# Performance work log

Hardware: AMD Instinct MI355X
Metric: run time of the kernel (lower is better)

Reference implementation:

```python
import jax, jax.numpy as jnp
import numpy as np

B = 262144      # batch of Monte Carlo paths
D = 5           # number of assets
NSTEPS = 20     # Euler-Maruyama steps
H = 0.1         # T / N
R = 0.06        # risk-free rate
T = 2.0
SIGMA = 0.2     # vol (same for all assets)
B_DRIFT = 0.1   # P-measure drift
CURTAGE = 0.005
SQRT_H = float(np.sqrt(H))


def setup_inputs() -> dict:
    key = jax.random.key(0)
    ks = jax.random.split(key, 10)
    sc = 0.1  # weight init scale
    return {
        "x_in": jax.random.uniform(ks[0], (B, 1), dtype=jnp.float32),
        "dW": jax.random.normal(ks[1], (NSTEPS, B, D), dtype=jnp.float32) * SQRT_H,
        "Wo": jax.random.normal(ks[2], (1, 2 * D + 1), dtype=jnp.float32) * sc,
        "bo": jnp.zeros((2 * D + 1,), jnp.float32),
        "Wk": jax.random.normal(ks[3], (1, 2 * D), dtype=jnp.float32) * sc,
        "bk": jnp.zeros((2 * D,), jnp.float32),
        "Wu0": jax.random.normal(ks[4], (1, D), dtype=jnp.float32) * sc,
        "bu0": jnp.zeros((D,), jnp.float32),
        "W1": jax.random.normal(ks[5], (NSTEPS - 1, 1, 20), dtype=jnp.float32) * sc,
        "b1": jnp.zeros((NSTEPS - 1, 20), jnp.float32),
        "W2": jax.random.normal(ks[6], (NSTEPS - 1, 20, 20), dtype=jnp.float32) * sc,
        "b2": jnp.zeros((NSTEPS - 1, 20), jnp.float32),
        "W3": jax.random.normal(ks[7], (NSTEPS - 1, 20, D), dtype=jnp.float32) * sc,
        "b3": jnp.zeros((NSTEPS - 1, D), jnp.float32),
    }


def _mlp(x, w1, c1, w2, c2, w3, c3):
    # SubNetwork: Dense(20) relu -> Dense(20) relu -> Dense(D) linear
    h1 = jax.nn.relu(x @ w1 + c1)
    h2 = jax.nn.relu(h1 @ w2 + c2)
    return h2 @ w3 + c3


def _forward(x_in, dW, Wo, bo, Wk, bk, Wu0, bu0, W1, b1, W2, b2, W3, b3):
    b_vec = jnp.full((D,), B_DRIFT, dtype=x_in.dtype)
    x = x_in                                             # wealth [B,1]
    alpha_options = jax.nn.softmax(x @ Wo + bo, axis=-1)[:, : 2 * D]
    alpha_options_tot = jnp.mean(jnp.sum(alpha_options, axis=1))
    K = 1.0 + 0.25 * jnp.tanh(x @ Wk + bk)               # strikes [B,2D]
    rescale = 1.0 - alpha_options_tot
    alpha = x @ Wu0 + bu0                                # linear head, [B,D]

    S = jnp.ones((x.shape[0], D), dtype=x.dtype)         # P-measure asset prices
    S_Q = S                                              # Q-measure asset prices
    dN_acu = jnp.zeros((x.shape[0], D), dtype=x.dtype)
    N_m1 = None

    for n in range(1, NSTEPS + 1):   # fixed small unrolled rollout
        u = alpha                                        # dollar allocation per asset
        N_p = u / S                                      # number of shares
        if n > 1:
            dN_acu = dN_acu + jnp.abs(N_p - N_m1)        # turnover accumulator
        N_m1 = N_p
        dWn = dW[n - 1]
        # wealth Euler step: risk-free on cash + risky exposure (GBM, no jumps)
        x = x + (x - jnp.sum(u, axis=1, keepdims=True)) * (R * H) \
              + jnp.sum(u * (b_vec * H + SIGMA * dWn), axis=1, keepdims=True)
        S = S * (1.0 + b_vec * H + SIGMA * dWn)
        S_Q = S_Q * (1.0 + R * H + SIGMA * dWn)
        if n < NSTEPS:
            alpha = _mlp(x, W1[n - 1], b1[n - 1], W2[n - 1], b2[n - 1],
                         W3[n - 1], b3[n - 1])

    dN = jnp.sum(dN_acu, axis=1, keepdims=True)          # [B,1]
    disc = jnp.exp(-R * T)
    C0 = disc * jnp.mean(jnp.maximum(S_Q - K[:, :D], 0.0), axis=0)   # [D] MC call price
    P0 = disc * jnp.mean(jnp.maximum(K[:, D:] - S_Q, 0.0), axis=0)   # [D] MC put price
    C_T = jnp.maximum(S - K[:, :D], 0.0) / (C0 + 1e-8)
    P_T = jnp.maximum(K[:, D:] - S, 0.0) / (P0 + 1e-8)
    del P_T  # options_in_p=False: puts/calls not added to wealth

    x = x - CURTAGE * dN                                 # transaction costs

    p5 = jnp.percentile(x, 5.0)
    p95 = jnp.percentile(x, 95.0)
    m_lo = x < p5
    m_hi = x > p95
    cnt_lo = jnp.maximum(jnp.sum(m_lo), 1).astype(x.dtype)
    cnt_hi = jnp.maximum(jnp.sum(m_hi), 1).astype(x.dtype)

    loss1 = -jnp.mean(x)
    loss2 = jnp.var(x)
    loss3 = -jnp.sum(jnp.where(m_lo, x, 0.0)) / cnt_lo   # -CVaR_5 tail mean
    loss4 = -jnp.sum(jnp.where(m_hi, x, 0.0)) / cnt_hi
    loss5 = jnp.mean(C_T[:, 0])
    loss6 = K[0, 1]
    loss7 = jnp.asarray(rescale, x.dtype)
    return (loss1, loss2, loss3, loss4, loss5, loss6, loss7)


def reference(x_in, dW, Wo, bo, Wk, bk, Wu0, bu0, W1, b1, W2, b2, W3, b3):
    losses = _forward(x_in, dW, Wo, bo, Wk, bk, Wu0, bu0,
                      W1, b1, W2, b2, W3, b3)
    return tuple(jnp.reshape(l, (1,)) for l in losses)
```

## Files before the change

kernel.cpp:

```cpp
#include <hip/hip_runtime.h>
#include <math.h>

#define BB 262144
#define NST 20
#define RHc 0.006f
#define BHc 0.01f
#define SIGc 0.2f
#define CURTc 0.005f
#define DISCf 0.8869204367171575f

#define P 4
#define THB 256
#define NBLK_SIM 256
#define CH 65536

#define H1_BLK 32
#define H1_THR 1024
#define W_BLK 256
#define W_THR 256

#define SIMP_OFF  BB
#define TAILP_OFF (SIMP_OFF + NBLK_SIM * 5)
#define ICTRL     (TAILP_OFF + W_BLK * 4)
#define H2_OFF 0
#define H3_OFF 8192
#define CNT_OFF 12288
#define ST_OFF  12296
#define SF_OFF  12320
#define ZTOT    12289
#define H1R_OFF 12352

__device__ __forceinline__ unsigned fkey(float f) {
    unsigned u = __float_as_uint(f);
    return (u & 0x80000000u) ? ~u : (u | 0x80000000u);
}
__device__ __forceinline__ float funkey(unsigned k) {
    return __uint_as_float((k & 0x80000000u) ? (k ^ 0x80000000u) : ~k);
}
__device__ __forceinline__ float wred(float v) {
#pragma unroll
    for (int o = 32; o > 0; o >>= 1) v += __shfl_down(v, o);
    return v;
}
__device__ __forceinline__ unsigned short f2bf(float f) {
    unsigned u = __float_as_uint(f);
    unsigned r = u + 0x7fffu + ((u >> 16) & 1u);
    return (unsigned short)(r >> 16);
}

__global__ void zero_kernel(int* __restrict__ ctrl) {
    int i = blockIdx.x * blockDim.x + threadIdx.x;
    if (i < ZTOT) ctrl[i] = 0;
}

#define STRD 416
#define HB   (19 * STRD)

__global__ __launch_bounds__(THB, 1) void sim_kernel(
    const float* __restrict__ x_in, const float* __restrict__ dW,
    const float* __restrict__ Wo, const float* __restrict__ bo,
    const float* __restrict__ Wk, const float* __restrict__ bk,
    const float* __restrict__ Wu0, const float* __restrict__ bu0,
    const float* __restrict__ W1, const float* __restrict__ b1,
    const float* __restrict__ W2, const float* __restrict__ b2,
    const float* __restrict__ W3, const float* __restrict__ b3,
    float* __restrict__ ws, int* __restrict__ ctrl, float* __restrict__ out)
{
    __shared__ float L[HB + 40];
    __shared__ float red[4][5];
    __shared__ int lastF;
    const int tid = threadIdx.x;

    for (int t = tid; t < 19 * 20; t += THB) {
        int s = t / 20, j = t % 20;
        L[s * STRD + j]      = W1[t];
        L[s * STRD + 20 + j] = b1[t];
        L[s * STRD + 40 + j] = b2[t];
    }
    for (int t = tid; t < 19 * 100; t += THB) {
        int s = t / 100, r = t % 100, i = r / 5, k = r % 5;
        L[s * STRD + 60 + k * 20 + i] = W3[t];
    }
    for (int t = tid; t < 19 * 5; t += THB) {
        int s = t / 5, k = t % 5;
        L[s * STRD + 160 + k] = b3[t];
    }
    {
        unsigned short* Ls16 = (unsigned short*)L;
        for (int t = tid; t < 19 * 400; t += THB) {
            int s = t / 400, r = t % 400, i = r / 20, j = r % 20;
            Ls16[(s * STRD + 168 + i * 12) * 2 + j] = f2bf(W2[t]);
        }
        for (int t = tid; t < 19 * 80; t += THB) {
            int s = t / 80, r = t % 80, i = r / 4, q = r % 4;
            Ls16[(s * STRD + 168 + i * 12) * 2 + 20 + q] = 0;
        }
    }
    if (tid < 11) { L[HB + tid] = Wo[tid]; L[HB + 11 + tid] = bo[tid]; }
    if (tid == 0) { L[HB + 22] = Wk[0]; L[HB + 23] = bk[0]; }
    if (tid < 5)  { L[HB + 24 + tid] = Wu0[tid]; L[HB + 29 + tid] = bu0[tid]; }
    __syncthreads();

    const int b0 = blockIdx.x * THB + tid;

    float x[P], K0[P], SQ0[P], dNs[P], smv = 0.f;
    float alpha[P][5], S[P][5], Nm1[P][5], dwb[P][5];

#pragma unroll
    for (int p = 0; p < P; p++) {
        int b = b0 + p * CH;
        float xx = x_in[b];
        x[p] = xx;
        float z[11], zm = -1e30f;
#pragma unroll
        for (int j = 0; j < 11; j++) {
            z[j] = fmaf(xx, L[HB + j], L[HB + 11 + j]);
            zm = fmaxf(zm, z[j]);
        }
        float se = 0.f;
#pragma unroll
        for (int j = 0; j < 11; j++) se += __expf(z[j] - zm);
        smv += __expf(z[10] - zm) / se;
        K0[p] = 1.f + 0.25f * tanhf(fmaf(xx, L[HB + 22], L[HB + 23]));
        SQ0[p] = 1.f; dNs[p] = 0.f;
#pragma unroll
        for (int d = 0; d < 5; d++) {
            alpha[p][d] = fmaf(xx, L[HB + 24 + d], L[HB + 29 + d]);
            S[p][d] = 1.f;
            Nm1[p][d] = alpha[p][d];
        }
        const float* pw = dW + (size_t)b * 5;
#pragma unroll
        for (int d = 0; d < 5; d++) dwb[p][d] = pw[d];
    }

#pragma unroll 1
    for (int n = 1; n <= NST; n++) {
        float dwc[P][5];
#pragma unroll
        for (int p = 0; p < P; p++)
#pragma unroll
            for (int d = 0; d < 5; d++) dwc[p][d] = dwb[p][d];
        if (n < NST) {
#pragma unroll
            for (int p = 0; p < P; p++) {
                const float* pw = dW + ((size_t)n * BB + b0 + p * CH) * 5;
#pragma unroll
                for (int d = 0; d < 5; d++) dwb[p][d] = pw[d];
            }
        }
#pragma unroll
        for (int p = 0; p < P; p++) {
            float usum = 0.f, du = 0.f, dn = 0.f;
#pragma unroll
            for (int d = 0; d < 5; d++) {
                float u = alpha[p][d];
                float Np = u * __builtin_amdgcn_rcpf(S[p][d]);
                dn += fabsf(Np - Nm1[p][d]);
                Nm1[p][d] = Np;
                usum += u;
                du = fmaf(u, fmaf(SIGc, dwc[p][d], BHc), du);
            }
            dNs[p] += dn;
            x[p] = fmaf(x[p] - usum, RHc, x[p]) + du;
#pragma unroll
            for (int d = 0; d < 5; d++)
                S[p][d] *= (1.f + BHc + SIGc * dwc[p][d]);
            SQ0[p] *= (1.f + RHc + SIGc * dwc[p][0]);
        }
        if (n < NST) {
            const float* Ls = L + (n - 1) * STRD;
            float h2[P][20];
#pragma unroll
            for (int j4 = 0; j4 < 5; j4++) {
                float4 c = *(const float4*)(Ls + 40 + j4 * 4);
#pragma unroll
                for (int p = 0; p < P; p++) {
                    h2[p][j4 * 4 + 0] = c.x; h2[p][j4 * 4 + 1] = c.y;
                    h2[p][j4 * 4 + 2] = c.z; h2[p][j4 * 4 + 3] = c.w;
                }
            }
#pragma unroll 1
            for (int i4 = 0; i4 < 5; i4++) {
                float4 w1c = *(const float4*)(Ls + i4 * 4);
                float4 c1c = *(const float4*)(Ls + 20 + i4 * 4);
#pragma unroll
                for (int ii = 0; ii < 4; ii++) {
                    int i = i4 * 4 + ii;
                    const uint4 q0 = *(const uint4*)(Ls + 168 + i * 12);
                    const uint4 q1 = *(const uint4*)(Ls + 168 + i * 12 + 4);
                    const uint2 q2 = *(const uint2*)(Ls + 168 + i * 12 + 8);
                    float w[20];
                    w[0]  = __uint_as_float(q0.x << 16); w[1]  = __uint_as_float(q0.x & 0xffff0000u);
                    w[2]  = __uint_as_float(q0.y << 16); w[3]  = __uint_as_float(q0.y & 0xffff0000u);
                    w[4]  = __uint_as_float(q0.z << 16); w[5]  = __uint_as_float(q0.z & 0xffff0000u);
                    w[6]  = __uint_as_float(q0.w << 16); w[7]  = __uint_as_float(q0.w & 0xffff0000u);
                    w[8]  = __uint_as_float(q1.x << 16); w[9]  = __uint_as_float(q1.x & 0xffff0000u);
                    w[10] = __uint_as_float(q1.y << 16); w[11] = __uint_as_float(q1.y & 0xffff0000u);
                    w[12] = __uint_as_float(q1.z << 16); w[13] = __uint_as_float(q1.z & 0xffff0000u);
                    w[14] = __uint_as_float(q1.w << 16); w[15] = __uint_as_float(q1.w & 0xffff0000u);
                    w[16] = __uint_as_float(q2.x << 16); w[17] = __uint_as_float(q2.x & 0xffff0000u);
                    w[18] = __uint_as_float(q2.y << 16); w[19] = __uint_as_float(q2.y & 0xffff0000u);
                    float wv = (ii == 0) ? w1c.x : (ii == 1) ? w1c.y : (ii == 2) ? w1c.z : w1c.w;
                    float cv = (ii == 0) ? c1c.x : (ii == 1) ? c1c.y : (ii == 2) ? c1c.z : c1c.w;
#pragma unroll
                    for (int p = 0; p < P; p++) {
                        float hv = fmaxf(fmaf(x[p], wv, cv), 0.f);
#pragma unroll
                        for (int j = 0; j < 20; j++)
                            h2[p][j] = fmaf(hv, w[j], h2[p][j]);
                    }
                }
            }
#pragma unroll
            for (int p = 0; p < P; p++)
#pragma unroll
                for (int j = 0; j < 20; j++) h2[p][j] = fmaxf(h2[p][j], 0.f);
#pragma unroll
            for (int k = 0; k < 5; k++) {
                const float* wr = Ls + 60 + k * 20;
                float4 wa  = *(const float4*)(wr + 0);
                float4 wb2 = *(const float4*)(wr + 4);
                float4 wc2 = *(const float4*)(wr + 8);
                float4 wd2 = *(const float4*)(wr + 12);
                float4 we2 = *(const float4*)(wr + 16);
                float bb = Ls[160 + k];
#pragma unroll
                for (int p = 0; p < P; p++) {
                    float a = bb;
                    a = fmaf(h2[p][0], wa.x, a);  a = fmaf(h2[p][1], wa.y, a);
                    a = fmaf(h2[p][2], wa.z, a);  a = fmaf(h2[p][3], wa.w, a);
                    a = fmaf(h2[p][4], wb2.x, a); a = fmaf(h2[p][5], wb2.y, a);
                    a = fmaf(h2[p][6], wb2.z, a); a = fmaf(h2[p][7], wb2.w, a);
                    a = fmaf(h2[p][8], wc2.x, a); a = fmaf(h2[p][9], wc2.y, a);
                    a = fmaf(h2[p][10], wc2.z, a); a = fmaf(h2[p][11], wc2.w, a);
                    a = fmaf(h2[p][12], wd2.x, a); a = fmaf(h2[p][13], wd2.y, a);
                    a = fmaf(h2[p][14], wd2.z, a); a = fmaf(h2[p][15], wd2.w, a);
                    a = fmaf(h2[p][16], we2.x, a); a = fmaf(h2[p][17], we2.y, a);
                    a = fmaf(h2[p][18], we2.z, a); a = fmaf(h2[p][19], we2.w, a);
                    alpha[p][k] = a;
                }
            }
        }
    }

    float v0 = 0.f, v1 = 0.f, v2 = 0.f, v3 = 0.f, v4 = smv;
#pragma unroll
    for (int p = 0; p < P; p++) {
        float xx = fmaf(-CURTc, dNs[p], x[p]);
        ws[b0 + p * CH] = xx;
        v0 += xx; v1 += xx * xx;
        v2 += fmaxf(S[p][0] - K0[p], 0.f);
        v3 += fmaxf(SQ0[p]  - K0[p], 0.f);
    }

    v0 = wred(v0); v1 = wred(v1); v2 = wred(v2); v3 = wred(v3); v4 = wred(v4);
    int wid = tid >> 6, lane = tid & 63;
    if (lane == 0) { red[wid][0] = v0; red[wid][1] = v1; red[wid][2] = v2; red[wid][3] = v3; red[wid][4] = v4; }
    __syncthreads();
    if (tid == 0) {
        float s0 = 0, s1 = 0, s2 = 0, s3 = 0, s4 = 0;
#pragma unroll
        for (int w = 0; w < 4; w++) { s0 += red[w][0]; s1 += red[w][1]; s2 += red[w][2]; s3 += red[w][3]; s4 += red[w][4]; }
        float* part = ws + SIMP_OFF + blockIdx.x * 5;
        part[0] = s0; part[1] = s1; part[2] = s2; part[3] = s3; part[4] = s4;
    }
    __threadfence();
    if (tid == 0) lastF = (atomicAdd(&ctrl[CNT_OFF], 1) == NBLK_SIM - 1);
    __syncthreads();
    if (!lastF) return;
    __threadfence();

    const float* part = ws + SIMP_OFF;
    float a0 = part[tid * 5 + 0], a1 = part[tid * 5 + 1], a2 = part[tid * 5 + 2],
          a3 = part[tid * 5 + 3], a4 = part[tid * 5 + 4];
    a0 = wred(a0); a1 = wred(a1); a2 = wred(a2); a3 = wred(a3); a4 = wred(a4);
    if (lane == 0) { red[wid][0] = a0; red[wid][1] = a1; red[wid][2] = a2; red[wid][3] = a3; red[wid][4] = a4; }
    __syncthreads();
    if (tid == 0) {
        float Sx = 0, Sx2 = 0, SP = 0, SQs = 0, Ssm = 0;
#pragma unroll
        for (int w = 0; w < 4; w++) { Sx += red[w][0]; Sx2 += red[w][1]; SP += red[w][2]; SQs += red[w][3]; Ssm += red[w][4]; }
        float invB = 1.f / (float)BB;
        float meanx = Sx * invB;
        out[0] = -meanx;
        out[1] = Sx2 * invB - meanx * meanx;
        out[4] = (SP * invB) / (DISCf * (SQs * invB) + 1e-8f);
        out[5] = 1.f + 0.25f * tanhf(fmaf(x_in[0], Wk[1], bk[1]));
        out[6] = Ssm * invB;
    }
}

__device__ __forceinline__ void aggAdd(int* h, int code) {
    bool act = (code >= 0);
    unsigned long long mask = __ballot(act);
    while (mask) {
        int leader = __ffsll((unsigned long long)mask) - 1;
        int lc = __shfl(code, leader);
        unsigned long long mm = __ballot(act && code == lc);
        if ((threadIdx.x & 63) == leader) atomicAdd(&h[lc], (int)__popcll(mm));
        mask &= ~mm;
    }
}

__device__ int excl_scan1024(int v, int tid, int* wsum) {
    __syncthreads();
    int lane = tid & 63, wid = tid >> 6;
    int inc = v;
#pragma unroll
    for (int o = 1; o < 64; o <<= 1) { int u = __shfl_up(inc, o); if (lane >= o) inc += u; }
    if (lane == 63) wsum[wid] = inc;
    __syncthreads();
    if (tid < 16) {
        int wv = wsum[tid], winc = wv;
#pragma unroll
        for (int o = 1; o < 16; o <<= 1) { int u = __shfl_up(winc, o); if (tid >= o) winc += u; }
        wsum[tid] = winc - wv;
    }
    __syncthreads();
    return wsum[wid] + inc - v;
}

__global__ __launch_bounds__(H1_THR) void hist1_kernel(const float* __restrict__ xf,
                                                       int* __restrict__ ctrl)
{
    __shared__ int lh[2048];
    const int tid = threadIdx.x, bl = blockIdx.x;
    for (int i = tid; i < 2048; i += H1_THR) lh[i] = 0;
    __syncthreads();
    const float4* xf4 = (const float4*)xf;
#pragma unroll
    for (int w = 0; w < 2; w++) {
        float4 v = xf4[(size_t)bl * 2048 + w * 1024 + tid];
        aggAdd(lh, (int)(fkey(v.x) >> 21));
        aggAdd(lh, (int)(fkey(v.y) >> 21));
        aggAdd(lh, (int)(fkey(v.z) >> 21));
        aggAdd(lh, (int)(fkey(v.w) >> 21));
    }
    __syncthreads();
    int* row = ctrl + H1R_OFF + bl * 2048;
    for (int i = tid; i < 2048; i += H1_THR) row[i] = lh[i];
}

__global__ __launch_bounds__(1024) void scan1_kernel(int* __restrict__ ctrl)
{
    __shared__ int wsum[16];
    __shared__ int binT[4], remT[4];
    const int tid = threadIdx.x;
    const int* rows = ctrl + H1R_OFF;
    int c0 = 0, c1 = 0;
    for (int r = 0; r < H1_BLK; r++) {
        c0 += rows[r * 2048 + 2 * tid];
        c1 += rows[r * 2048 + 2 * tid + 1];
    }
    int s = c0 + c1;
    int E = excl_scan1024(s, tid, wsum);
    const int RK[4] = {13107, 13108, 249035, 249036};
#pragma unroll
    for (int t = 0; t < 4; t++) {
        int r = RK[t];
        if (r >= E && r < E + s) {
            if (r < E + c0) { binT[t] = 2 * tid;     remT[t] = r - E; }
            else            { binT[t] = 2 * tid + 1; remT[t] = r - E - c0; }
        }
    }
    __syncthreads();
    if (tid == 0) {
        for (int t = 0; t < 4; t++) { ctrl[ST_OFF + t] = binT[t]; ctrl[ST_OFF + 4 + t] = remT[t]; }
        for (int t = 0; t < 4; t++) {
            int g = t;
            for (int q = 0; q < t; q++) if (binT[q] == binT[t]) { g = q; break; }
            ctrl[ST_OFF + 8 + t] = g;
        }
    }
}

__global__ __launch_bounds__(W_THR) void hist2_kernel(const float* __restrict__ xf,
                                                      int* __restrict__ ctrl)
{
    const int tid = threadIdx.x, bl = blockIdx.x;
    int pf[4], gp[4];
#pragma unroll
    for (int t = 0; t < 4; t++) { pf[t] = ctrl[ST_OFF + t]; gp[t] = ctrl[ST_OFF + 8 + t]; }
    float4 v = ((const float4*)xf)[(size_t)bl * W_THR + tid];
    float xv[4] = {v.x, v.y, v.z, v.w};
#pragma unroll
    for (int k = 0; k < 4; k++) {
        unsigned u = fkey(xv[k]);
        unsigned hi = u >> 21;
        int bin = (int)((u >> 10) & 2047u);
        int code = -1;
#pragma unroll
        for (int t = 0; t < 4; t++)
            if (gp[t] == t && (unsigned)pf[t] == hi) code = t * 2048 + bin;
        aggAdd(ctrl + H2_OFF, code);
    }
}

__global__ __launch_bounds__(1024) void scan2_kernel(int* __restrict__ ctrl)
{
    __shared__ int wsum[16];
    __shared__ int binT[4], remT[4];
    const int tid = threadIdx.x;
    for (int t = 0; t < 4; t++) {
        int g = ctrl[ST_OFF + 8 + t], rank = ctrl[ST_OFF + 4 + t];
        const int* h = ctrl + H2_OFF + g * 2048;
        int c0 = h[2 * tid], c1 = h[2 * tid + 1];
        int s = c0 + c1;
        int E = excl_scan1024(s, tid, wsum);
        if (rank >= E && rank < E + s) {
            if (rank < E + c0) { binT[t] = 2 * tid;     remT[t] = rank - E; }
            else               { binT[t] = 2 * tid + 1; remT[t] = rank - E - c0; }
        }
        __syncthreads();
    }
    if (tid == 0) {
        int P2n[4];
        for (int t = 0; t < 4; t++) {
            P2n[t] = (ctrl[ST_OFF + t] << 11) | binT[t];
            ctrl[ST_OFF + 12 + t] = P2n[t];
            ctrl[ST_OFF + 16 + t] = remT[t];
        }
        for (int t = 0; t < 4; t++) {
            int g = t;
            for (int q = 0; q < t; q++) if (P2n[q] == P2n[t]) { g = q; break; }
            ctrl[ST_OFF + 20 + t] = g;
        }
    }
}

__global__ __launch_bounds__(W_THR) void hist3_kernel(const float* __restrict__ xf,
                                                      int* __restrict__ ctrl)
{
    const int tid = threadIdx.x, bl = blockIdx.x;
    int pf[4], gp[4];
#pragma unroll
    for (int t = 0; t < 4; t++) { pf[t] = ctrl[ST_OFF + 12 + t]; gp[t] = ctrl[ST_OFF + 20 + t]; }
    float4 v = ((const float4*)xf)[(size_t)bl * W_THR + tid];
    float xv[4] = {v.x, v.y, v.z, v.w};
#pragma unroll
    for (int k = 0; k < 4; k++) {
        unsigned u = fkey(xv[k]);
        unsigned hi = u >> 10;
        int bin = (int)(u & 1023u);
        int code = -1;
#pragma unroll
        for (int t = 0; t < 4; t++)
            if (gp[t] == t && (unsigned)pf[t] == hi) code = t * 1024 + bin;
        aggAdd(ctrl + H3_OFF, code);
    }
}

__global__ __launch_bounds__(1024) void scan3_kernel(int* __restrict__ ctrl)
{
    __shared__ int wsum[16];
    __shared__ int binT[4];
    const int tid = threadIdx.x;
    for (int t = 0; t < 4; t++) {
        int g = ctrl[ST_OFF + 20 + t], rank = ctrl[ST_OFF + 16 + t];
        const int* h = ctrl + H3_OFF + g * 1024;
        int s = h[tid];
        int E = excl_scan1024(s, tid, wsum);
        if (rank >= E && rank < E + s) binT[t] = tid;
        __syncthreads();
    }
    if (tid == 0) {
        float* sf = (float*)(ctrl + SF_OFF);
        float v[4];
        for (int t = 0; t < 4; t++) {
            unsigned key = ((unsigned)ctrl[ST_OFF + 12 + t] << 10) | (unsigned)binT[t];
            v[t] = funkey(key);
            sf[t] = v[t];
        }
        sf[4] = v[0] + 0.15f * (v[1] - v[0]);
        sf[5] = v[2] + 0.85f * (v[3] - v[2]);
    }
}

__global__ __launch_bounds__(W_THR) void tail_kernel(const float* __restrict__ xf,
                                                     const int* __restrict__ ctrl,
                                                     float* __restrict__ ws)
{
    __shared__ float frd[4][4];
    const int tid = threadIdx.x, bl = blockIdx.x;
    const float* sf = (const float*)(ctrl + SF_OFF);
    const float p5 = sf[4], p95 = sf[5];
    float4 v = ((const float4*)xf)[(size_t)bl * W_THR + tid];
    float xv[4] = {v.x, v.y, v.z, v.w};
    float slo = 0.f, clo = 0.f, shi = 0.f, chi = 0.f;
#pragma unroll
    for (int k = 0; k < 4; k++) {
        float x = xv[k];
        if (x < p5)  { slo += x; clo += 1.f; }
        if (x > p95) { shi += x; chi += 1.f; }
    }
    slo = wred(slo); clo = wred(clo); shi = wred(shi); chi = wred(chi);
    int wid = tid >> 6, lane = tid & 63;
    if (lane == 0) { frd[wid][0] = slo; frd[wid][1] = clo; frd[wid][2] = shi; frd[wid][3] = chi; }
    __syncthreads();
    if (tid == 0) {
        float s0 = 0, s1 = 0, s2 = 0, s3 = 0;
#pragma unroll
        for (int w = 0; w < 4; w++) { s0 += frd[w][0]; s1 += frd[w][1]; s2 += frd[w][2]; s3 += frd[w][3]; }
        float* tp = ws + TAILP_OFF + bl * 4;
        tp[0] = s0; tp[1] = s1; tp[2] = s2; tp[3] = s3;
    }
}

__global__ __launch_bounds__(256) void tailfin_kernel(const float* __restrict__ ws,
                                                      float* __restrict__ out)
{
    __shared__ float frd[4][4];
    const int tid = threadIdx.x;
    const float* tp = ws + TAILP_OFF;
    float a0 = tp[tid * 4 + 0], a1 = tp[tid * 4 + 1], a2 = tp[tid * 4 + 2], a3 = tp[tid * 4 + 3];
    a0 = wred(a0); a1 = wred(a1); a2 = wred(a2); a3 = wred(a3);
    int wid = tid >> 6, lane = tid & 63;
    if (lane == 0) { frd[wid][0] = a0; frd[wid][1] = a1; frd[wid][2] = a2; frd[wid][3] = a3; }
    __syncthreads();
    if (tid == 0) {
        float Slo = 0, Clo = 0, Shi = 0, Chi = 0;
#pragma unroll
        for (int w = 0; w < 4; w++) { Slo += frd[w][0]; Clo += frd[w][1]; Shi += frd[w][2]; Chi += frd[w][3]; }
        out[2] = -Slo / fmaxf(Clo, 1.f);
        out[3] = -Shi / fmaxf(Chi, 1.f);
    }
}

extern "C" void kernel_launch(void* const* d_in, const int* in_sizes, int n_in,
                              void* d_out, int out_size, void* d_ws, size_t ws_size,
                              hipStream_t stream)
{
    const float* x_in = (const float*)d_in[0];
    const float* dW   = (const float*)d_in[1];
    const float* Wo   = (const float*)d_in[2];
    const float* bo   = (const float*)d_in[3];
    const float* Wk   = (const float*)d_in[4];
    const float* bk   = (const float*)d_in[5];
    const float* Wu0  = (const float*)d_in[6];
    const float* bu0  = (const float*)d_in[7];
    const float* W1   = (const float*)d_in[8];
    const float* b1   = (const float*)d_in[9];
    const float* W2   = (const float*)d_in[10];
    const float* b2   = (const float*)d_in[11];
    const float* W3   = (const float*)d_in[12];
    const float* b3   = (const float*)d_in[13];
    float* ws  = (float*)d_ws;
    int* ctrl  = (int*)d_ws + ICTRL;
    float* out = (float*)d_out;

    zero_kernel<<<(ZTOT + 1023) / 1024, 1024, 0, stream>>>(ctrl);
    sim_kernel<<<NBLK_SIM, THB, 0, stream>>>(x_in, dW, Wo, bo, Wk, bk, Wu0, bu0,
                                             W1, b1, W2, b2, W3, b3, ws, ctrl, out);
    hist1_kernel<<<H1_BLK, H1_THR, 0, stream>>>(ws, ctrl);
    scan1_kernel<<<1, 1024, 0, stream>>>(ctrl);
    hist2_kernel<<<W_BLK, W_THR, 0, stream>>>(ws, ctrl);
    scan2_kernel<<<1, 1024, 0, stream>>>(ctrl);
    hist3_kernel<<<W_BLK, W_THR, 0, stream>>>(ws, ctrl);
    scan3_kernel<<<1, 1024, 0, stream>>>(ctrl);
    tail_kernel<<<W_BLK, W_THR, 0, stream>>>(ws, ctrl, ws);
    tailfin_kernel<<<1, 256, 0, stream>>>(ws, out);
}
```

Baseline: 192.1 us.

## Run per-step MLP layers on bf16 MFMA with pre-packed weight fragments

The per-path scalar FMA MLP (20x20 and 20x5 layers in LDS-bf16) is replaced by 32x32x16 bf16 MFMA instructions, with two half-waves splitting the five asset dimensions. A new prep kernel packs W2/W3/biases into MFMA fragment layouts in global memory, and the sim kernel now uses one path per lane-pair with many more blocks instead of four paths per thread. Hidden activations are also rounded to bf16, which adds precision loss, and the extra kernel launch and wider grid change the reduction and histogram partitioning.

```diff
diff --git a/kernel.cpp b/kernel.cpp
--- a/kernel.cpp
+++ b/kernel.cpp
@@ -1,4 +1,5 @@
 #include <hip/hip_runtime.h>
+#include <hip/hip_bf16.h>
 #include <math.h>
 
 #define BB 262144
@@ -9,12 +10,9 @@
 #define CURTc 0.005f
 #define DISCf 0.8869204367171575f
 
-#define P 4
 #define THB 256
-#define NBLK_SIM 256
-#define CH 65536
-
-#define H1_BLK 32
+#define NBLK_SIM 2048
+#define H1_BLK 16
 #define H1_THR 1024
 #define W_BLK 256
 #define W_THR 256
@@ -29,7 +27,22 @@
 #define SF_OFF  12320
 #define ZTOT    12289
 #define H1R_OFF 12352
-
+#define PREP_OFF (ICTRL + H1R_OFF)
+#define PSTR 1152
+#define HEADO (19 * PSTR)
+
+typedef float f32x16 __attribute__((ext_vector_type(16)));
+typedef short bf16x8 __attribute__((ext_vector_type(8)));
+union F8  { int4 i; bf16x8 b; };
+union BFR { int u[4]; bf16x8 b; };
+union C16 { float4 f4[4]; f32x16 v; };
+
+__device__ __forceinline__ unsigned pkbf(float lo, float hi) {
+    __hip_bfloat162 t = __float22bfloat162_rn(make_float2(lo, hi));
+    unsigned r;
+    __builtin_memcpy(&r, &t, 4);
+    return r;
+}
 __device__ __forceinline__ unsigned fkey(float f) {
     unsigned u = __float_as_uint(f);
     return (u & 0x80000000u) ? ~u : (u | 0x80000000u);
@@ -53,206 +66,181 @@
     if (i < ZTOT) ctrl[i] = 0;
 }
 
-#define STRD 416
-#define HB   (19 * STRD)
-
-__global__ __launch_bounds__(THB, 1) void sim_kernel(
+__global__ void prep_kernel(const float* __restrict__ Wu0, const float* __restrict__ bu0,
+                            const float* __restrict__ W1, const float* __restrict__ b1,
+                            const float* __restrict__ W2, const float* __restrict__ b2,
+                            const float* __restrict__ W3, const float* __restrict__ b3,
+                            float* __restrict__ prepF)
+{
+    const int s = blockIdx.x, tid = threadIdx.x;
+    int* prepI = (int*)prepF;
+    if (s < 19) {
+        for (int t = tid; t < 512; t += 256) {
+            int c = t >> 8, l = (t >> 2) & 63, v = t & 3;
+            int g = l >> 5, row = l & 31;
+            int kb = 16 * c + 8 * (v >> 1) + 4 * g + 2 * (v & 1);
+            float lo = (row < 20 && kb     < 20) ? W2[s * 400 + kb * 20 + row]       : 0.f;
+            float hi = (row < 20 && kb + 1 < 20) ? W2[s * 400 + (kb + 1) * 20 + row] : 0.f;
+            prepI[s * PSTR + c * 256 + l * 4 + v] = (int)(((unsigned)f2bf(hi) << 16) | f2bf(lo));
+            float lo3 = (row < 5 && kb     < 20) ? W3[s * 100 + kb * 5 + row]       : 0.f;
+            float hi3 = (row < 5 && kb + 1 < 20) ? W3[s * 100 + (kb + 1) * 5 + row] : 0.f;
+            prepI[s * PSTR + 512 + c * 256 + l * 4 + v] = (int)(((unsigned)f2bf(hi3) << 16) | f2bf(lo3));
+        }
+        if (tid < 48) {
+            int g = tid / 24, j0 = tid % 24, j = j0 % 12;
+            int n = (j < 4) ? 4 * g + j : (j < 8) ? 8 + 4 * g + (j - 4) : 16 + 4 * g + (j - 8);
+            float val = 0.f;
+            if (n < 20) val = (j0 >= 12) ? b1[s * 20 + n] : W1[s * 20 + n];
+            prepF[s * PSTR + 1024 + g * 24 + j0] = val;
+        }
+        if (tid < 32) {
+            int g = tid >> 4, r = tid & 15;
+            int row = (r & 3) + 8 * (r >> 2) + 4 * g;
+            prepF[s * PSTR + 1072 + tid] = (row < 20) ? b2[s * 20 + row] : 0.f;
+            prepF[s * PSTR + 1104 + tid] = (row < 5)  ? b3[s * 5 + row]  : 0.f;
+        }
+    } else {
+        if (tid < 8) {
+            int g = tid >> 2, r = tid & 3, d = r + 4 * g;
+            prepF[HEADO + tid]     = (d < 5) ? Wu0[d] : 0.f;
+            prepF[HEADO + 8 + tid] = (d < 5) ? bu0[d] : 0.f;
+        }
+    }
+}
+
+__global__ __launch_bounds__(THB, 2) void sim_kernel(
     const float* __restrict__ x_in, const float* __restrict__ dW,
     const float* __restrict__ Wo, const float* __restrict__ bo,
     const float* __restrict__ Wk, const float* __restrict__ bk,
-    const float* __restrict__ Wu0, const float* __restrict__ bu0,
-    const float* __restrict__ W1, const float* __restrict__ b1,
-    const float* __restrict__ W2, const float* __restrict__ b2,
-    const float* __restrict__ W3, const float* __restrict__ b3,
-    float* __restrict__ ws, int* __restrict__ ctrl, float* __restrict__ out)
-{
-    __shared__ float L[HB + 40];
+    float* __restrict__ ws, int* __restrict__ ctrl, float* __restrict__ out,
+    const float* __restrict__ prepF)
+{
     __shared__ float red[4][5];
     __shared__ int lastF;
     const int tid = threadIdx.x;
-
-    for (int t = tid; t < 19 * 20; t += THB) {
-        int s = t / 20, j = t % 20;
-        L[s * STRD + j]      = W1[t];
-        L[s * STRD + 20 + j] = b1[t];
-        L[s * STRD + 40 + j] = b2[t];
-    }
-    for (int t = tid; t < 19 * 100; t += THB) {
-        int s = t / 100, r = t % 100, i = r / 5, k = r % 5;
-        L[s * STRD + 60 + k * 20 + i] = W3[t];
-    }
-    for (int t = tid; t < 19 * 5; t += THB) {
-        int s = t / 5, k = t % 5;
-        L[s * STRD + 160 + k] = b3[t];
-    }
+    const int l = tid & 63;
+    const int g = l >> 5;
+    const bool gm = (g == 0);
+    const int p = blockIdx.x * 128 + (tid >> 6) * 32 + (l & 31);
+
+    float x = x_in[p];
+
+    float z[11], zm = -1e30f;
+#pragma unroll
+    for (int j = 0; j < 11; j++) {
+        z[j] = fmaf(x, Wo[j], bo[j]);
+        zm = fmaxf(zm, z[j]);
+    }
+    float se = 0.f;
+#pragma unroll
+    for (int j = 0; j < 11; j++) se += __expf(z[j] - zm);
+    float smv = __expf(z[10] - zm) / se;
+
+    float K0 = 1.f + 0.25f * tanhf(fmaf(x, Wk[0], bk[0]));
+
+    float a[4];
     {
-        unsigned short* Ls16 = (unsigned short*)L;
-        for (int t = tid; t < 19 * 400; t += THB) {
-            int s = t / 400, r = t % 400, i = r / 20, j = r % 20;
-            Ls16[(s * STRD + 168 + i * 12) * 2 + j] = f2bf(W2[t]);
-        }
-        for (int t = tid; t < 19 * 80; t += THB) {
-            int s = t / 80, r = t % 80, i = r / 4, q = r % 4;
-            Ls16[(s * STRD + 168 + i * 12) * 2 + 20 + q] = 0;
-        }
-    }
-    if (tid < 11) { L[HB + tid] = Wo[tid]; L[HB + 11 + tid] = bo[tid]; }
-    if (tid == 0) { L[HB + 22] = Wk[0]; L[HB + 23] = bk[0]; }
-    if (tid < 5)  { L[HB + 24 + tid] = Wu0[tid]; L[HB + 29 + tid] = bu0[tid]; }
-    __syncthreads();
-
-    const int b0 = blockIdx.x * THB + tid;
-
-    float x[P], K0[P], SQ0[P], dNs[P], smv = 0.f;
-    float alpha[P][5], S[P][5], Nm1[P][5], dwb[P][5];
-
-#pragma unroll
-    for (int p = 0; p < P; p++) {
-        int b = b0 + p * CH;
-        float xx = x_in[b];
-        x[p] = xx;
-        float z[11], zm = -1e30f;
-#pragma unroll
-        for (int j = 0; j < 11; j++) {
-            z[j] = fmaf(xx, L[HB + j], L[HB + 11 + j]);
-            zm = fmaxf(zm, z[j]);
-        }
-        float se = 0.f;
-#pragma unroll
-        for (int j = 0; j < 11; j++) se += __expf(z[j] - zm);
-        smv += __expf(z[10] - zm) / se;
-        K0[p] = 1.f + 0.25f * tanhf(fmaf(xx, L[HB + 22], L[HB + 23]));
-        SQ0[p] = 1.f; dNs[p] = 0.f;
-#pragma unroll
-        for (int d = 0; d < 5; d++) {
-            alpha[p][d] = fmaf(xx, L[HB + 24 + d], L[HB + 29 + d]);
-            S[p][d] = 1.f;
-            Nm1[p][d] = alpha[p][d];
-        }
-        const float* pw = dW + (size_t)b * 5;
-#pragma unroll
-        for (int d = 0; d < 5; d++) dwb[p][d] = pw[d];
+        float4 w4 = *(const float4*)(prepF + HEADO + g * 4);
+        float4 b4 = *(const float4*)(prepF + HEADO + 8 + g * 4);
+        a[0] = fmaf(x, w4.x, b4.x); a[1] = fmaf(x, w4.y, b4.y);
+        a[2] = fmaf(x, w4.z, b4.z); a[3] = fmaf(x, w4.w, b4.w);
+    }
+    float S[4] = {1.f, 1.f, 1.f, 1.f}, Nm1[4], dwb[4];
+    float SQ0 = 1.f, dNs = 0.f;
+#pragma unroll
+    for (int e = 0; e < 4; e++) Nm1[e] = a[e];
+
+    {
+        const float* pw = dW + (size_t)p * 5;
+        float d0 = pw[0], d1 = pw[1], d2v = pw[2], d3v = pw[3], d4 = pw[4];
+        dwb[0] = gm ? d0 : d4;
+        dwb[1] = gm ? d1 : 0.f; dwb[2] = gm ? d2v : 0.f; dwb[3] = gm ? d3v : 0.f;
     }
 
 #pragma unroll 1
     for (int n = 1; n <= NST; n++) {
-        float dwc[P][5];
-#pragma unroll
-        for (int p = 0; p < P; p++)
-#pragma unroll
-            for (int d = 0; d < 5; d++) dwc[p][d] = dwb[p][d];
+        float dwc[4];
+#pragma unroll
+        for (int e = 0; e < 4; e++) dwc[e] = dwb[e];
         if (n < NST) {
-#pragma unroll
-            for (int p = 0; p < P; p++) {
-                const float* pw = dW + ((size_t)n * BB + b0 + p * CH) * 5;
-#pragma unroll
-                for (int d = 0; d < 5; d++) dwb[p][d] = pw[d];
+            const float* pw = dW + ((size_t)n * BB + p) * 5;
+            float d0 = pw[0], d1 = pw[1], d2v = pw[2], d3v = pw[3], d4 = pw[4];
+            dwb[0] = gm ? d0 : d4;
+            dwb[1] = gm ? d1 : 0.f; dwb[2] = gm ? d2v : 0.f; dwb[3] = gm ? d3v : 0.f;
+        }
+        float du = 0.f, us = 0.f;
+#pragma unroll
+        for (int e = 0; e < 4; e++) {
+            float f = fmaf(SIGc, dwc[e], BHc);
+            du = fmaf(a[e], f, du);
+            us += a[e];
+            float Np = a[e] * __builtin_amdgcn_rcpf(S[e]);
+            dNs += fabsf(Np - Nm1[e]);
+            Nm1[e] = Np;
+            S[e] = fmaf(S[e], f, S[e]);
+        }
+        SQ0 = fmaf(SQ0, fmaf(SIGc, dwc[0], RHc), SQ0);
+        du += __shfl_xor(du, 32);
+        us += __shfl_xor(us, 32);
+        x = fmaf(x - us, RHc, x) + du;
+
+        if (n < NST) {
+            const float* sb = prepF + (n - 1) * PSTR;
+            const float4* lw = (const float4*)(sb + 1024 + g * 24);
+            float4 wA = lw[0], wB = lw[1], wC = lw[2];
+            float4 bA = lw[3], bB = lw[4], bC = lw[5];
+            float h[12];
+            h[0]  = fmaxf(fmaf(x, wA.x, bA.x), 0.f); h[1]  = fmaxf(fmaf(x, wA.y, bA.y), 0.f);
+            h[2]  = fmaxf(fmaf(x, wA.z, bA.z), 0.f); h[3]  = fmaxf(fmaf(x, wA.w, bA.w), 0.f);
+            h[4]  = fmaxf(fmaf(x, wB.x, bB.x), 0.f); h[5]  = fmaxf(fmaf(x, wB.y, bB.y), 0.f);
+            h[6]  = fmaxf(fmaf(x, wB.z, bB.z), 0.f); h[7]  = fmaxf(fmaf(x, wB.w, bB.w), 0.f);
+            h[8]  = fmaxf(fmaf(x, wC.x, bC.x), 0.f); h[9]  = fmaxf(fmaf(x, wC.y, bC.y), 0.f);
+            h[10] = fmaxf(fmaf(x, wC.z, bC.z), 0.f); h[11] = fmaxf(fmaf(x, wC.w, bC.w), 0.f);
+            BFR b1c0, b1c1;
+            b1c0.u[0] = pkbf(h[0], h[1]);  b1c0.u[1] = pkbf(h[2], h[3]);
+            b1c0.u[2] = pkbf(h[4], h[5]);  b1c0.u[3] = pkbf(h[6], h[7]);
+            b1c1.u[0] = pkbf(h[8], h[9]);  b1c1.u[1] = pkbf(h[10], h[11]);
+            b1c1.u[2] = 0;                 b1c1.u[3] = 0;
+            F8 A2c0, A2c1;
+            const int4* a2p = (const int4*)sb + l;
+            A2c0.i = a2p[0]; A2c1.i = a2p[64];
+            C16 c2;
+            {
+                const float4* bp = (const float4*)(sb + 1072 + g * 16);
+                c2.f4[0] = bp[0]; c2.f4[1] = bp[1]; c2.f4[2] = bp[2]; c2.f4[3] = bp[3];
             }
-        }
-#pragma unroll
-        for (int p = 0; p < P; p++) {
-            float usum = 0.f, du = 0.f, dn = 0.f;
-#pragma unroll
-            for (int d = 0; d < 5; d++) {
-                float u = alpha[p][d];
-                float Np = u * __builtin_amdgcn_rcpf(S[p][d]);
-                dn += fabsf(Np - Nm1[p][d]);
-                Nm1[p][d] = Np;
-                usum += u;
-                du = fmaf(u, fmaf(SIGc, dwc[p][d], BHc), du);
+            f32x16 d2 = __builtin_amdgcn_mfma_f32_32x32x16_bf16(A2c0.b, b1c0.b, c2.v, 0, 0, 0);
+            d2 = __builtin_amdgcn_mfma_f32_32x32x16_bf16(A2c1.b, b1c1.b, d2, 0, 0, 0);
+            float h2r[12];
+#pragma unroll
+            for (int i = 0; i < 12; i++) h2r[i] = fmaxf(d2[i], 0.f);
+            BFR b2c0, b2c1;
+            b2c0.u[0] = pkbf(h2r[0], h2r[1]); b2c0.u[1] = pkbf(h2r[2], h2r[3]);
+            b2c0.u[2] = pkbf(h2r[4], h2r[5]); b2c0.u[3] = pkbf(h2r[6], h2r[7]);
+            b2c1.u[0] = pkbf(h2r[8], h2r[9]); b2c1.u[1] = pkbf(h2r[10], h2r[11]);
+            b2c1.u[2] = 0;                    b2c1.u[3] = 0;
+            F8 A3c0, A3c1;
+            const int4* a3p = (const int4*)(sb + 512) + l;
+            A3c0.i = a3p[0]; A3c1.i = a3p[64];
+            C16 c3;
+            {
+                const float4* bp = (const float4*)(sb + 1104 + g * 16);
+                c3.f4[0] = bp[0]; c3.f4[1] = bp[1]; c3.f4[2] = bp[2]; c3.f4[3] = bp[3];
             }
-            dNs[p] += dn;
-            x[p] = fmaf(x[p] - usum, RHc, x[p]) + du;
-#pragma unroll
-            for (int d = 0; d < 5; d++)
-                S[p][d] *= (1.f + BHc + SIGc * dwc[p][d]);
-            SQ0[p] *= (1.f + RHc + SIGc * dwc[p][0]);
-        }
-        if (n < NST) {
-            const float* Ls = L + (n - 1) * STRD;
-            float h2[P][20];
-#pragma unroll
-            for (int j4 = 0; j4 < 5; j4++) {
-                float4 c = *(const float4*)(Ls + 40 + j4 * 4);
-#pragma unroll
-                for (int p = 0; p < P; p++) {
-                    h2[p][j4 * 4 + 0] = c.x; h2[p][j4 * 4 + 1] = c.y;
-                    h2[p][j4 * 4 + 2] = c.z; h2[p][j4 * 4 + 3] = c.w;
-                }
-            }
-#pragma unroll 1
-            for (int i4 = 0; i4 < 5; i4++) {
-                float4 w1c = *(const float4*)(Ls + i4 * 4);
-                float4 c1c = *(const float4*)(Ls + 20 + i4 * 4);
-#pragma unroll
-                for (int ii = 0; ii < 4; ii++) {
-                    int i = i4 * 4 + ii;
-                    const uint4 q0 = *(const uint4*)(Ls + 168 + i * 12);
-                    const uint4 q1 = *(const uint4*)(Ls + 168 + i * 12 + 4);
-                    const uint2 q2 = *(const uint2*)(Ls + 168 + i * 12 + 8);
-                    float w[20];
-                    w[0]  = __uint_as_float(q0.x << 16); w[1]  = __uint_as_float(q0.x & 0xffff0000u);
-                    w[2]  = __uint_as_float(q0.y << 16); w[3]  = __uint_as_float(q0.y & 0xffff0000u);
-                    w[4]  = __uint_as_float(q0.z << 16); w[5]  = __uint_as_float(q0.z & 0xffff0000u);
-                    w[6]  = __uint_as_float(q0.w << 16); w[7]  = __uint_as_float(q0.w & 0xffff0000u);
-                    w[8]  = __uint_as_float(q1.x << 16); w[9]  = __uint_as_float(q1.x & 0xffff0000u);
-                    w[10] = __uint_as_float(q1.y << 16); w[11] = __uint_as_float(q1.y & 0xffff0000u);
-                    w[12] = __uint_as_float(q1.z << 16); w[13] = __uint_as_float(q1.z & 0xffff0000u);
-                    w[14] = __uint_as_float(q1.w << 16); w[15] = __uint_as_float(q1.w & 0xffff0000u);
-                    w[16] = __uint_as_float(q2.x << 16); w[17] = __uint_as_float(q2.x & 0xffff0000u);
-                    w[18] = __uint_as_float(q2.y << 16); w[19] = __uint_as_float(q2.y & 0xffff0000u);
-                    float wv = (ii == 0) ? w1c.x : (ii == 1) ? w1c.y : (ii == 2) ? w1c.z : w1c.w;
-                    float cv = (ii == 0) ? c1c.x : (ii == 1) ? c1c.y : (ii == 2) ? c1c.z : c1c.w;
-#pragma unroll
-                    for (int p = 0; p < P; p++) {
-                        float hv = fmaxf(fmaf(x[p], wv, cv), 0.f);
-#pragma unroll
-                        for (int j = 0; j < 20; j++)
-                            h2[p][j] = fmaf(hv, w[j], h2[p][j]);
-                    }
-                }
-            }
-#pragma unroll
-            for (int p = 0; p < P; p++)
-#pragma unroll
-                for (int j = 0; j < 20; j++) h2[p][j] = fmaxf(h2[p][j], 0.f);
-#pragma unroll
-            for (int k = 0; k < 5; k++) {
-                const float* wr = Ls + 60 + k * 20;
-                float4 wa  = *(const float4*)(wr + 0);
-                float4 wb2 = *(const float4*)(wr + 4);
-                float4 wc2 = *(const float4*)(wr + 8);
-                float4 wd2 = *(const float4*)(wr + 12);
-                float4 we2 = *(const float4*)(wr + 16);
-                float bb = Ls[160 + k];
-#pragma unroll
-                for (int p = 0; p < P; p++) {
-                    float a = bb;
-                    a = fmaf(h2[p][0], wa.x, a);  a = fmaf(h2[p][1], wa.y, a);
-                    a = fmaf(h2[p][2], wa.z, a);  a = fmaf(h2[p][3], wa.w, a);
-                    a = fmaf(h2[p][4], wb2.x, a); a = fmaf(h2[p][5], wb2.y, a);
-                    a = fmaf(h2[p][6], wb2.z, a); a = fmaf(h2[p][7], wb2.w, a);
-                    a = fmaf(h2[p][8], wc2.x, a); a = fmaf(h2[p][9], wc2.y, a);
-                    a = fmaf(h2[p][10], wc2.z, a); a = fmaf(h2[p][11], wc2.w, a);
-                    a = fmaf(h2[p][12], wd2.x, a); a = fmaf(h2[p][13], wd2.y, a);
-                    a = fmaf(h2[p][14], wd2.z, a); a = fmaf(h2[p][15], wd2.w, a);
-                    a = fmaf(h2[p][16], we2.x, a); a = fmaf(h2[p][17], we2.y, a);
-                    a = fmaf(h2[p][18], we2.z, a); a = fmaf(h2[p][19], we2.w, a);
-                    alpha[p][k] = a;
-                }
-            }
-        }
-    }
-
-    float v0 = 0.f, v1 = 0.f, v2 = 0.f, v3 = 0.f, v4 = smv;
-#pragma unroll
-    for (int p = 0; p < P; p++) {
-        float xx = fmaf(-CURTc, dNs[p], x[p]);
-        ws[b0 + p * CH] = xx;
-        v0 += xx; v1 += xx * xx;
-        v2 += fmaxf(S[p][0] - K0[p], 0.f);
-        v3 += fmaxf(SQ0[p]  - K0[p], 0.f);
-    }
+            f32x16 d3 = __builtin_amdgcn_mfma_f32_32x32x16_bf16(A3c0.b, b2c0.b, c3.v, 0, 0, 0);
+            d3 = __builtin_amdgcn_mfma_f32_32x32x16_bf16(A3c1.b, b2c1.b, d3, 0, 0, 0);
+            a[0] = d3[0]; a[1] = d3[1]; a[2] = d3[2]; a[3] = d3[3];
+        }
+    }
+
+    float dnO = __shfl_xor(dNs, 32);
+    float xx = fmaf(-CURTc, dNs + dnO, x);
+    if (gm) ws[p] = xx;
+    float v0 = gm ? xx : 0.f;
+    float v1 = gm ? xx * xx : 0.f;
+    float v2 = gm ? fmaxf(S[0] - K0, 0.f) : 0.f;
+    float v3 = gm ? fmaxf(SQ0 - K0, 0.f) : 0.f;
+    float v4 = gm ? smv : 0.f;
 
     v0 = wred(v0); v1 = wred(v1); v2 = wred(v2); v3 = wred(v3); v4 = wred(v4);
     int wid = tid >> 6, lane = tid & 63;
@@ -272,8 +260,11 @@
     __threadfence();
 
     const float* part = ws + SIMP_OFF;
-    float a0 = part[tid * 5 + 0], a1 = part[tid * 5 + 1], a2 = part[tid * 5 + 2],
-          a3 = part[tid * 5 + 3], a4 = part[tid * 5 + 4];
+    float a0 = 0, a1 = 0, a2 = 0, a3 = 0, a4 = 0;
+    for (int r = tid; r < NBLK_SIM; r += THB) {
+        const float* pr = part + r * 5;
+        a0 += pr[0]; a1 += pr[1]; a2 += pr[2]; a3 += pr[3]; a4 += pr[4];
+    }
     a0 = wred(a0); a1 = wred(a1); a2 = wred(a2); a3 = wred(a3); a4 = wred(a4);
     if (lane == 0) { red[wid][0] = a0; red[wid][1] = a1; red[wid][2] = a2; red[wid][3] = a3; red[wid][4] = a4; }
     __syncthreads();
@@ -330,8 +321,8 @@
     __syncthreads();
     const float4* xf4 = (const float4*)xf;
 #pragma unroll
-    for (int w = 0; w < 2; w++) {
-        float4 v = xf4[(size_t)bl * 2048 + w * 1024 + tid];
+    for (int w = 0; w < 4; w++) {
+        float4 v = xf4[(size_t)bl * 4096 + w * 1024 + tid];
         aggAdd(lh, (int)(fkey(v.x) >> 21));
         aggAdd(lh, (int)(fkey(v.y) >> 21));
         aggAdd(lh, (int)(fkey(v.z) >> 21));
@@ -545,13 +536,14 @@
     const float* b2   = (const float*)d_in[11];
     const float* W3   = (const float*)d_in[12];
     const float* b3   = (const float*)d_in[13];
-    float* ws  = (float*)d_ws;
-    int* ctrl  = (int*)d_ws + ICTRL;
-    float* out = (float*)d_out;
+    float* ws   = (float*)d_ws;
+    int* ctrl   = (int*)d_ws + ICTRL;
+    float* prep = ws + PREP_OFF;
+    float* out  = (float*)d_out;
 
     zero_kernel<<<(ZTOT + 1023) / 1024, 1024, 0, stream>>>(ctrl);
-    sim_kernel<<<NBLK_SIM, THB, 0, stream>>>(x_in, dW, Wo, bo, Wk, bk, Wu0, bu0,
-                                             W1, b1, W2, b2, W3, b3, ws, ctrl, out);
+    prep_kernel<<<20, 256, 0, stream>>>(Wu0, bu0, W1, b1, W2, b2, W3, b3, prep);
+    sim_kernel<<<NBLK_SIM, THB, 0, stream>>>(x_in, dW, Wo, bo, Wk, bk, ws, ctrl, out, prep);
     hist1_kernel<<<H1_BLK, H1_THR, 0, stream>>>(ws, ctrl);
     scan1_kernel<<<1, 1024, 0, stream>>>(ctrl);
     hist2_kernel<<<W_BLK, W_THR, 0, stream>>>(ws, ctrl);
```

New measurement: 352.7 us. 1.84x slower.
